# Performance work log

Measured on AMD Instinct MI355X. Metric: run time of the kernel, lower is better.

The kernel has to match this reference:

```python
import jax, jax.numpy as jnp
import numpy as np

T = 10       # Newton-Schulz iterations (module init arg)
EPS = 1e-05  # ridge added to covariance


def setup_inputs() -> dict:
    key = jax.random.key(0)
    # [B, C, H, W] feature map fed into the concept-whitening layer
    X = jax.random.normal(key, (128, 256, 28, 28), dtype=jnp.float32)
    return {"X": X}


def _iternorm_whiten(X):
    """Training-mode IterNorm whitening (g=1 group): ZCA via Newton-Schulz."""
    B, C, H, W = X.shape
    # X.transpose(0,1).view(C, -1): channels-first flatten -> [C, m], m = B*H*W
    x = jnp.moveaxis(X, 0, 1).reshape(C, -1)
    m = x.shape[-1]
    mean = x.mean(-1, keepdims=True)                      # [C, 1]
    xc = x - mean                                         # [C, m]
    I = jnp.eye(C, dtype=X.dtype)
    # Sigma = eps*I + (1/m) * xc @ xc^T
    Sigma = EPS * I + (xc @ xc.T) * (1.0 / m)             # [C, C]
    rTr = 1.0 / jnp.trace(Sigma)                          # scalar
    Sigma_N = Sigma * rTr                                 # trace-normalized

    def newton_step(P, _):
        # P_{k+1} = 1.5*P_k - 0.5 * P_k^3 @ Sigma_N
        P3 = P @ P @ P
        return 1.5 * P - 0.5 * (P3 @ Sigma_N), None

    P, _ = jax.lax.scan(newton_step, I, None, length=T)
    wm = P * jnp.sqrt(rTr)                                # whitening matrix [C, C]
    xn = wm @ xc                                          # [C, m]
    # reshape back: view(C, B, H, W).transpose(0, 1) -> [B, C, H, W]
    return jnp.moveaxis(xn.reshape(C, B, H, W), 0, 1)


def reference(X):
    # IterNormRotation.forward with mode=-1 (default): X_hat = IterNorm.apply(X, ...)
    # The concept-alignment branch (mode >= 0) runs under no_grad and is skipped.
    return _iternorm_whiten(X)
```

## Files before the change

kernel.cpp:

```cpp
#include <hip/hip_runtime.h>


#define HW 784
#define BHW 200704
#define INV_M (1.0f/100352.0f)
#define EPS_RIDGE 1e-5f

typedef __bf16 bf8 __attribute__((ext_vector_type(8)));
typedef float  f4  __attribute__((ext_vector_type(4)));

__device__ __forceinline__ f4 mfma16(bf8 a, bf8 b, f4 c){
  return __builtin_amdgcn_mfma_f32_16x16x32_bf16(a, b, c, 0, 0, 0);
}

__device__ __forceinline__ unsigned short f2bf_rne(float f){
  unsigned u = __builtin_bit_cast(unsigned, f);
  return (unsigned short)((u + 0x7fffu + ((u >> 16) & 1u)) >> 16);
}
__device__ __forceinline__ float bf2f(unsigned short h){
  unsigned u = ((unsigned)h) << 16;
  return __builtin_bit_cast(float, u);
}
__device__ __forceinline__ void split_bf(float f, unsigned short& h, unsigned short& l){
  h = f2bf_rne(f);
  float r = f - bf2f(h);
  l = f2bf_rne(r);
}

__global__ __launch_bounds__(512, 2) void cov_kernel(const float* __restrict__ X,
                                                     float* __restrict__ part,
                                                     float* __restrict__ chansum){
  __shared__ unsigned short Ah[256][40];
  __shared__ unsigned short Al[256][40];
  __shared__ float ssum[256];
  const int t = threadIdx.x;
  const int blk = blockIdx.x;
  const int b = blk >> 1;
  const int h = blk & 1;
  const int base_hw = h * 400;
  const int len    = h ? 384 : 400;
  const int nsteps = h ? 12  : 13;
  const float* __restrict__ Xb = X + (size_t)b * BHW;

  if (t < 256) ssum[t] = 0.0f;

  const int lane = t & 63;
  const int wave = t >> 6;
  const int wm = wave >> 2;
  const int wn = wave & 3;
  const int lr = lane & 15;
  const int ko = lane >> 4;

  f4 acc[8][4];
  #pragma unroll
  for (int m = 0; m < 8; m++)
    #pragma unroll
    for (int n = 0; n < 4; n++) acc[m][n] = f4{0.f, 0.f, 0.f, 0.f};

  float csum[4] = {0.f, 0.f, 0.f, 0.f};
  const int srow = t >> 3;
  const int sfq  = t & 7;

  for (int ks = 0; ks < nsteps; ++ks){
    if (ks) __syncthreads();
    #pragma unroll
    for (int i = 0; i < 4; i++){
      int row = srow + i * 64;
      int hwl = ks * 32 + sfq * 4;
      float4 v = make_float4(0.f, 0.f, 0.f, 0.f);
      if (hwl < len) v = *(const float4*)&Xb[(size_t)row * HW + base_hw + hwl];
      csum[i] += v.x + v.y + v.z + v.w;
      unsigned short h0,l0,h1,l1,h2,l2,h3,l3;
      split_bf(v.x, h0, l0); split_bf(v.y, h1, l1);
      split_bf(v.z, h2, l2); split_bf(v.w, h3, l3);
      *(ushort4*)&Ah[row][sfq * 4] = make_ushort4(h0, h1, h2, h3);
      *(ushort4*)&Al[row][sfq * 4] = make_ushort4(l0, l1, l2, l3);
    }
    __syncthreads();
    bf8 bhf[4], blf[4];
    #pragma unroll
    for (int n = 0; n < 4; n++){
      int coln = wn * 64 + n * 16 + lr;
      bhf[n] = *(const bf8*)&Ah[coln][ko * 8];
      blf[n] = *(const bf8*)&Al[coln][ko * 8];
    }
    #pragma unroll
    for (int m = 0; m < 8; m++){
      int rowm = wm * 128 + m * 16 + lr;
      bf8 ahf = *(const bf8*)&Ah[rowm][ko * 8];
      bf8 alf = *(const bf8*)&Al[rowm][ko * 8];
      #pragma unroll
      for (int n = 0; n < 4; n++){
        acc[m][n] = mfma16(ahf, bhf[n], acc[m][n]);
        acc[m][n] = mfma16(ahf, blf[n], acc[m][n]);
        acc[m][n] = mfma16(alf, bhf[n], acc[m][n]);
      }
    }
  }
  atomicAdd(&ssum[srow      ], csum[0]);
  atomicAdd(&ssum[srow +  64], csum[1]);
  atomicAdd(&ssum[srow + 128], csum[2]);
  atomicAdd(&ssum[srow + 192], csum[3]);
  __syncthreads();
  if (t < 256) atomicAdd(&chansum[t], ssum[t]);

  float* __restrict__ Pp = part + (size_t)blk * 65536;
  const int cr4 = (lane >> 4) * 4;
  #pragma unroll
  for (int m = 0; m < 8; m++){
    #pragma unroll
    for (int n = 0; n < 4; n++){
      int colw = wn * 64 + n * 16 + lr;
      #pragma unroll
      for (int r = 0; r < 4; r++){
        int roww = wm * 128 + m * 16 + cr4 + r;
        Pp[roww * 256 + colw] = acc[m][n][r];
      }
    }
  }
}

__global__ __launch_bounds__(256) void reduce_kernel(const float* __restrict__ part,
                                                     const float* __restrict__ chansum,
                                                     float* __restrict__ Sig,
                                                     float* __restrict__ trace){
  const int i = blockIdx.x;
  const int j = threadIdx.x;
  float s = 0.f;
  #pragma unroll 8
  for (int p = 0; p < 256; p++) s += part[(size_t)p * 65536 + i * 256 + j];
  float mi = chansum[i] * INV_M;
  float mj = chansum[j] * INV_M;
  float v = s * INV_M - mi * mj + ((i == j) ? EPS_RIDGE : 0.f);
  Sig[i * 256 + j] = v;
  if (i == j) atomicAdd(trace, v);
}

__global__ __launch_bounds__(256) void prep_kernel(const float* __restrict__ Sig,
                                                   const float* __restrict__ trace,
                                                   float* __restrict__ SigN,
                                                   float* __restrict__ P1){
  const int idx = blockIdx.x * 256 + threadIdx.x;
  const float rTr = 1.0f / trace[0];
  const float sn = Sig[idx] * rTr;
  SigN[idx] = sn;
  const int i = idx >> 8, j = idx & 255;
  P1[idx] = ((i == j) ? 1.5f : 0.0f) - 0.5f * sn;
}

__global__ __launch_bounds__(256) void mm256_kernel(const float* __restrict__ A,
                                                    const float* __restrict__ B0,
                                                    const float* __restrict__ B1,
                                                    float* __restrict__ O0,
                                                    float* __restrict__ O1,
                                                    const float* __restrict__ E,
                                                    float alpha, float beta){
  const float* __restrict__ B = blockIdx.z ? B1 : B0;
  float* __restrict__ O = blockIdx.z ? O1 : O0;
  __shared__ unsigned short Ah[64][40], Al[64][40], Bh[64][40], Bl[64][40];
  const int t = threadIdx.x;
  const int lane = t & 63;
  const int wave = t >> 6;
  const int wm = wave >> 1, wn = wave & 1;
  const int lr = lane & 15, ko = lane >> 4;
  const int r0 = blockIdx.x * 64, c0 = blockIdx.y * 64;
  f4 acc[2][2];
  acc[0][0] = f4{0.f,0.f,0.f,0.f}; acc[0][1] = f4{0.f,0.f,0.f,0.f};
  acc[1][0] = f4{0.f,0.f,0.f,0.f}; acc[1][1] = f4{0.f,0.f,0.f,0.f};

  for (int ks = 0; ks < 8; ++ks){
    if (ks) __syncthreads();
    #pragma unroll
    for (int i = 0; i < 2; i++){
      int idx = i * 256 + t;
      int row = idx >> 3, fq = idx & 7;
      float4 v = *(const float4*)&A[(r0 + row) * 256 + ks * 32 + fq * 4];
      unsigned short h0,l0,h1,l1,h2,l2,h3,l3;
      split_bf(v.x, h0, l0); split_bf(v.y, h1, l1);
      split_bf(v.z, h2, l2); split_bf(v.w, h3, l3);
      *(ushort4*)&Ah[row][fq * 4] = make_ushort4(h0, h1, h2, h3);
      *(ushort4*)&Al[row][fq * 4] = make_ushort4(l0, l1, l2, l3);
    }
    #pragma unroll
    for (int i = 0; i < 2; i++){
      int idx = i * 256 + t;
      int k = idx >> 4, cq = idx & 15;
      float4 v = *(const float4*)&B[(ks * 32 + k) * 256 + c0 + cq * 4];
      unsigned short hh, ll;
      split_bf(v.x, hh, ll); Bh[cq*4+0][k] = hh; Bl[cq*4+0][k] = ll;
      split_bf(v.y, hh, ll); Bh[cq*4+1][k] = hh; Bl[cq*4+1][k] = ll;
      split_bf(v.z, hh, ll); Bh[cq*4+2][k] = hh; Bl[cq*4+2][k] = ll;
      split_bf(v.w, hh, ll); Bh[cq*4+3][k] = hh; Bl[cq*4+3][k] = ll;
    }
    __syncthreads();
    #pragma unroll
    for (int m = 0; m < 2; m++){
      bf8 ahf = *(const bf8*)&Ah[wm * 32 + m * 16 + lr][ko * 8];
      bf8 alf = *(const bf8*)&Al[wm * 32 + m * 16 + lr][ko * 8];
      #pragma unroll
      for (int n = 0; n < 2; n++){
        bf8 bhf = *(const bf8*)&Bh[wn * 32 + n * 16 + lr][ko * 8];
        bf8 blf = *(const bf8*)&Bl[wn * 32 + n * 16 + lr][ko * 8];
        acc[m][n] = mfma16(ahf, bhf, acc[m][n]);
        acc[m][n] = mfma16(ahf, blf, acc[m][n]);
        acc[m][n] = mfma16(alf, bhf, acc[m][n]);
      }
    }
  }
  const int cr4 = (lane >> 4) * 4;
  #pragma unroll
  for (int m = 0; m < 2; m++)
    #pragma unroll
    for (int n = 0; n < 2; n++)
      #pragma unroll
      for (int r = 0; r < 4; r++){
        int row = r0 + wm * 32 + m * 16 + cr4 + r;
        int col = c0 + wn * 32 + n * 16 + lr;
        float v = alpha * acc[m][n][r];
        if (beta != 0.0f) v += beta * E[row * 256 + col];
        O[row * 256 + col] = v;
      }
}

__global__ __launch_bounds__(256) void wmprep_kernel(const float* __restrict__ P,
                                                     const float* __restrict__ trace,
                                                     const float* __restrict__ chansum,
                                                     unsigned short* __restrict__ wmhi,
                                                     unsigned short* __restrict__ wmlo,
                                                     float* __restrict__ woff){
  const int i = blockIdx.x, t = threadIdx.x;
  __shared__ float red[256];
  const float s = sqrtf(1.0f / trace[0]);
  float v = P[i * 256 + t] * s;
  unsigned short h, l;
  split_bf(v, h, l);
  wmhi[i * 256 + t] = h;
  wmlo[i * 256 + t] = l;
  red[t] = v * (chansum[t] * INV_M);
  __syncthreads();
  for (int st = 128; st > 0; st >>= 1){
    if (t < st) red[t] += red[t + st];
    __syncthreads();
  }
  if (t == 0) woff[i] = red[0];
}

__global__ __launch_bounds__(512, 2) void whiten_kernel(const float* __restrict__ X,
                                                        const unsigned short* __restrict__ wmhi,
                                                        const unsigned short* __restrict__ wmlo,
                                                        const float* __restrict__ woff,
                                                        float* __restrict__ out){
  __shared__ unsigned short Ahs[256][40], Als[256][40];
  __shared__ unsigned short Bhs[112][40], Bls[112][40];
  const int blk = blockIdx.x;
  const int b = blk / 7;
  const int ch = blk % 7;
  const int hw0 = ch * 112;
  const int t = threadIdx.x;
  const int lane = t & 63;
  const int wave = t >> 6;
  const int lr = lane & 15, ko = lane >> 4;
  const float* __restrict__ Xb = X + (size_t)b * BHW;
  f4 acc[2][7];
  #pragma unroll
  for (int m = 0; m < 2; m++)
    #pragma unroll
    for (int n = 0; n < 7; n++) acc[m][n] = f4{0.f, 0.f, 0.f, 0.f};

  const int arow = t >> 1, aseg = t & 1;
  for (int ks = 0; ks < 8; ++ks){
    if (ks) __syncthreads();
    {
      const uint4* sh = (const uint4*)(wmhi + arow * 256 + ks * 32 + aseg * 16);
      uint4 v0 = sh[0], v1 = sh[1];
      *(uint4*)&Ahs[arow][aseg * 16]     = v0;
      *(uint4*)&Ahs[arow][aseg * 16 + 8] = v1;
      const uint4* sl = (const uint4*)(wmlo + arow * 256 + ks * 32 + aseg * 16);
      uint4 w0 = sl[0], w1 = sl[1];
      *(uint4*)&Als[arow][aseg * 16]     = w0;
      *(uint4*)&Als[arow][aseg * 16 + 8] = w1;
    }
    #pragma unroll
    for (int i = 0; i < 2; i++){
      int idx = i * 512 + t;
      if (idx < 896){
        int k = idx / 28, q = idx % 28;
        float4 v = *(const float4*)&Xb[(size_t)(ks * 32 + k) * HW + hw0 + q * 4];
        unsigned short hh, ll;
        split_bf(v.x, hh, ll); Bhs[q*4+0][k] = hh; Bls[q*4+0][k] = ll;
        split_bf(v.y, hh, ll); Bhs[q*4+1][k] = hh; Bls[q*4+1][k] = ll;
        split_bf(v.z, hh, ll); Bhs[q*4+2][k] = hh; Bls[q*4+2][k] = ll;
        split_bf(v.w, hh, ll); Bhs[q*4+3][k] = hh; Bls[q*4+3][k] = ll;
      }
    }
    __syncthreads();
    bf8 bhf[7], blf[7];
    #pragma unroll
    for (int n = 0; n < 7; n++){
      bhf[n] = *(const bf8*)&Bhs[n * 16 + lr][ko * 8];
      blf[n] = *(const bf8*)&Bls[n * 16 + lr][ko * 8];
    }
    #pragma unroll
    for (int m = 0; m < 2; m++){
      bf8 ahf = *(const bf8*)&Ahs[wave * 32 + m * 16 + lr][ko * 8];
      bf8 alf = *(const bf8*)&Als[wave * 32 + m * 16 + lr][ko * 8];
      #pragma unroll
      for (int n = 0; n < 7; n++){
        acc[m][n] = mfma16(ahf, bhf[n], acc[m][n]);
        acc[m][n] = mfma16(ahf, blf[n], acc[m][n]);
        acc[m][n] = mfma16(alf, bhf[n], acc[m][n]);
      }
    }
  }
  const int cr4 = (lane >> 4) * 4;
  #pragma unroll
  for (int m = 0; m < 2; m++){
    #pragma unroll
    for (int r = 0; r < 4; r++){
      int c = wave * 32 + m * 16 + cr4 + r;
      float wofc = woff[c];
      #pragma unroll
      for (int n = 0; n < 7; n++){
        int hw = hw0 + n * 16 + lr;
        out[(size_t)b * BHW + (size_t)c * HW + hw] = acc[m][n][r] - wofc;
      }
    }
  }
}

extern "C" void kernel_launch(void* const* d_in, const int* in_sizes, int n_in,
                              void* d_out, int out_size, void* d_ws, size_t ws_size,
                              hipStream_t stream){
  const float* X = (const float*)d_in[0];
  float* out = (float*)d_out;
  char* ws = (char*)d_ws;
  float* part    = (float*)(ws);
  float* chansum = (float*)(ws + 67108864);
  float* trace   = (float*)(ws + 67108864 + 1024);
  float* Sig     = (float*)(ws + 67110912);
  float* SigN    = (float*)(ws + 67373056);
  float* Pa      = (float*)(ws + 67635200);
  float* Pb      = (float*)(ws + 67897344);
  float* C1      = (float*)(ws + 68159488);
  float* C2      = (float*)(ws + 68421632);
  float* woff    = (float*)(ws + 68683776);
  unsigned short* wmhi = (unsigned short*)(ws + 68685824);
  unsigned short* wmlo = (unsigned short*)(ws + 68816896);

  hipMemsetAsync(ws + 67108864, 0, 2048, stream);
  cov_kernel   <<<256, 512, 0, stream>>>(X, part, chansum);
  reduce_kernel<<<256, 256, 0, stream>>>(part, chansum, Sig, trace);
  prep_kernel  <<<256, 256, 0, stream>>>(Sig, trace, SigN, Pa);

  float* P = Pa; float* Pn = Pb;
  for (int it = 0; it < 9; ++it){
    mm256_kernel<<<dim3(4,4,2), 256, 0, stream>>>(P, P, SigN, C1, C2, nullptr, 1.0f, 0.0f);
    mm256_kernel<<<dim3(4,4,1), 256, 0, stream>>>(C1, C2, nullptr, Pn, nullptr, P, -0.5f, 1.5f);
    float* tmp = P; P = Pn; Pn = tmp;
  }

  wmprep_kernel<<<256, 256, 0, stream>>>(P, trace, chansum, wmhi, wmlo, woff);
  whiten_kernel<<<896, 512, 0, stream>>>(X, wmhi, wmlo, woff, out);
}
```

Measured before the change: 617.9 us.

## Load NS matmul operands row-wise via symmetry and transpose whiten tiles with shuffles

```diff
diff --git a/kernel.cpp b/kernel.cpp
--- a/kernel.cpp
+++ b/kernel.cpp
@@ -148,62 +148,59 @@
   P1[idx] = ((i == j) ? 1.5f : 0.0f) - 0.5f * sn;
 }
 
-__global__ __launch_bounds__(256) void mm256_kernel(const float* __restrict__ A,
-                                                    const float* __restrict__ B0,
-                                                    const float* __restrict__ B1,
-                                                    float* __restrict__ O0,
-                                                    float* __restrict__ O1,
-                                                    const float* __restrict__ E,
-                                                    float alpha, float beta){
+__global__ __launch_bounds__(256) void ns64_kernel(const float* __restrict__ A,
+                                                   const float* __restrict__ B0,
+                                                   const float* __restrict__ B1,
+                                                   float* __restrict__ O0,
+                                                   float* __restrict__ O1,
+                                                   const float* __restrict__ E,
+                                                   float alpha, float beta){
   const float* __restrict__ B = blockIdx.z ? B1 : B0;
   float* __restrict__ O = blockIdx.z ? O1 : O0;
-  __shared__ unsigned short Ah[64][40], Al[64][40], Bh[64][40], Bl[64][40];
+  __shared__ unsigned short Ah[64][136], Al[64][136], Bh[64][136], Bl[64][136];
   const int t = threadIdx.x;
   const int lane = t & 63;
   const int wave = t >> 6;
   const int wm = wave >> 1, wn = wave & 1;
   const int lr = lane & 15, ko = lane >> 4;
   const int r0 = blockIdx.x * 64, c0 = blockIdx.y * 64;
+  const int srow = t >> 2;
+  const int sc0 = (t & 3) * 32;
   f4 acc[2][2];
   acc[0][0] = f4{0.f,0.f,0.f,0.f}; acc[0][1] = f4{0.f,0.f,0.f,0.f};
   acc[1][0] = f4{0.f,0.f,0.f,0.f}; acc[1][1] = f4{0.f,0.f,0.f,0.f};
 
-  for (int ks = 0; ks < 8; ++ks){
-    if (ks) __syncthreads();
-    #pragma unroll
-    for (int i = 0; i < 2; i++){
-      int idx = i * 256 + t;
-      int row = idx >> 3, fq = idx & 7;
-      float4 v = *(const float4*)&A[(r0 + row) * 256 + ks * 32 + fq * 4];
+  for (int kh = 0; kh < 2; ++kh){
+    if (kh) __syncthreads();
+    #pragma unroll
+    for (int i = 0; i < 8; i++){
+      int col = sc0 + i * 4;
+      int gcol = kh * 128 + col;
       unsigned short h0,l0,h1,l1,h2,l2,h3,l3;
-      split_bf(v.x, h0, l0); split_bf(v.y, h1, l1);
-      split_bf(v.z, h2, l2); split_bf(v.w, h3, l3);
-      *(ushort4*)&Ah[row][fq * 4] = make_ushort4(h0, h1, h2, h3);
-      *(ushort4*)&Al[row][fq * 4] = make_ushort4(l0, l1, l2, l3);
-    }
-    #pragma unroll
-    for (int i = 0; i < 2; i++){
-      int idx = i * 256 + t;
-      int k = idx >> 4, cq = idx & 15;
-      float4 v = *(const float4*)&B[(ks * 32 + k) * 256 + c0 + cq * 4];
-      unsigned short hh, ll;
-      split_bf(v.x, hh, ll); Bh[cq*4+0][k] = hh; Bl[cq*4+0][k] = ll;
-      split_bf(v.y, hh, ll); Bh[cq*4+1][k] = hh; Bl[cq*4+1][k] = ll;
-      split_bf(v.z, hh, ll); Bh[cq*4+2][k] = hh; Bl[cq*4+2][k] = ll;
-      split_bf(v.w, hh, ll); Bh[cq*4+3][k] = hh; Bl[cq*4+3][k] = ll;
+      float4 va = *(const float4*)&A[(r0 + srow) * 256 + gcol];
+      split_bf(va.x,h0,l0); split_bf(va.y,h1,l1); split_bf(va.z,h2,l2); split_bf(va.w,h3,l3);
+      *(ushort4*)&Ah[srow][col] = make_ushort4(h0,h1,h2,h3);
+      *(ushort4*)&Al[srow][col] = make_ushort4(l0,l1,l2,l3);
+      float4 vb = *(const float4*)&B[(c0 + srow) * 256 + gcol];
+      split_bf(vb.x,h0,l0); split_bf(vb.y,h1,l1); split_bf(vb.z,h2,l2); split_bf(vb.w,h3,l3);
+      *(ushort4*)&Bh[srow][col] = make_ushort4(h0,h1,h2,h3);
+      *(ushort4*)&Bl[srow][col] = make_ushort4(l0,l1,l2,l3);
     }
     __syncthreads();
     #pragma unroll
-    for (int m = 0; m < 2; m++){
-      bf8 ahf = *(const bf8*)&Ah[wm * 32 + m * 16 + lr][ko * 8];
-      bf8 alf = *(const bf8*)&Al[wm * 32 + m * 16 + lr][ko * 8];
-      #pragma unroll
-      for (int n = 0; n < 2; n++){
-        bf8 bhf = *(const bf8*)&Bh[wn * 32 + n * 16 + lr][ko * 8];
-        bf8 blf = *(const bf8*)&Bl[wn * 32 + n * 16 + lr][ko * 8];
-        acc[m][n] = mfma16(ahf, bhf, acc[m][n]);
-        acc[m][n] = mfma16(ahf, blf, acc[m][n]);
-        acc[m][n] = mfma16(alf, bhf, acc[m][n]);
+    for (int ks = 0; ks < 4; ++ks){
+      #pragma unroll
+      for (int m = 0; m < 2; m++){
+        bf8 ahf = *(const bf8*)&Ah[wm * 32 + m * 16 + lr][ks * 32 + ko * 8];
+        bf8 alf = *(const bf8*)&Al[wm * 32 + m * 16 + lr][ks * 32 + ko * 8];
+        #pragma unroll
+        for (int n = 0; n < 2; n++){
+          bf8 bhf = *(const bf8*)&Bh[wn * 32 + n * 16 + lr][ks * 32 + ko * 8];
+          bf8 blf = *(const bf8*)&Bl[wn * 32 + n * 16 + lr][ks * 32 + ko * 8];
+          acc[m][n] = mfma16(ahf, bhf, acc[m][n]);
+          acc[m][n] = mfma16(ahf, blf, acc[m][n]);
+          acc[m][n] = mfma16(alf, bhf, acc[m][n]);
+        }
       }
     }
   }
@@ -268,6 +265,8 @@
     for (int n = 0; n < 7; n++) acc[m][n] = f4{0.f, 0.f, 0.f, 0.f};
 
   const int arow = t >> 1, aseg = t & 1;
+  const int g = lane >> 4;
+  const int cc = (t >> 4);
   for (int ks = 0; ks < 8; ++ks){
     if (ks) __syncthreads();
     {
@@ -281,16 +280,28 @@
       *(uint4*)&Als[arow][aseg * 16 + 8] = w1;
     }
     #pragma unroll
-    for (int i = 0; i < 2; i++){
-      int idx = i * 512 + t;
-      if (idx < 896){
-        int k = idx / 28, q = idx % 28;
-        float4 v = *(const float4*)&Xb[(size_t)(ks * 32 + k) * HW + hw0 + q * 4];
-        unsigned short hh, ll;
-        split_bf(v.x, hh, ll); Bhs[q*4+0][k] = hh; Bls[q*4+0][k] = ll;
-        split_bf(v.y, hh, ll); Bhs[q*4+1][k] = hh; Bls[q*4+1][k] = ll;
-        split_bf(v.z, hh, ll); Bhs[q*4+2][k] = hh; Bls[q*4+2][k] = ll;
-        split_bf(v.w, hh, ll); Bhs[q*4+3][k] = hh; Bls[q*4+3][k] = ll;
+    for (int p = 0; p < 2; p++){
+      int qh = p * 16 + (t & 15);
+      if (qh < 28){
+        float4 v = *(const float4*)&Xb[(size_t)(ks * 32 + cc) * HW + hw0 + qh * 4];
+        float r0 = __shfl_xor((g & 1) ? v.x : v.y, 16);
+        float r1 = __shfl_xor((g & 1) ? v.z : v.w, 16);
+        float a0 = (g & 1) ? r0  : v.x;
+        float a1 = (g & 1) ? v.y : r0;
+        float a2 = (g & 1) ? r1  : v.z;
+        float a3 = (g & 1) ? v.w : r1;
+        float s0 = __shfl_xor((g & 2) ? a0 : a2, 32);
+        float s1 = __shfl_xor((g & 2) ? a1 : a3, 32);
+        float b0v = (g & 2) ? s0 : a0;
+        float b1v = (g & 2) ? s1 : a1;
+        float b2v = (g & 2) ? a2 : s0;
+        float b3v = (g & 2) ? a3 : s1;
+        int row = qh * 4 + g;
+        int colk = (t >> 6) * 4;
+        unsigned short h0,l0,h1,l1,h2,l2,h3,l3;
+        split_bf(b0v,h0,l0); split_bf(b1v,h1,l1); split_bf(b2v,h2,l2); split_bf(b3v,h3,l3);
+        *(ushort4*)&Bhs[row][colk] = make_ushort4(h0,h1,h2,h3);
+        *(ushort4*)&Bls[row][colk] = make_ushort4(l0,l1,l2,l3);
       }
     }
     __syncthreads();
@@ -354,8 +365,8 @@
 
   float* P = Pa; float* Pn = Pb;
   for (int it = 0; it < 9; ++it){
-    mm256_kernel<<<dim3(4,4,2), 256, 0, stream>>>(P, P, SigN, C1, C2, nullptr, 1.0f, 0.0f);
-    mm256_kernel<<<dim3(4,4,1), 256, 0, stream>>>(C1, C2, nullptr, Pn, nullptr, P, -0.5f, 1.5f);
+    ns64_kernel<<<dim3(4,4,2), 256, 0, stream>>>(P, P, SigN, C1, C2, nullptr, 1.0f, 0.0f);
+    ns64_kernel<<<dim3(4,4,1), 256, 0, stream>>>(C1, C2, nullptr, Pn, nullptr, P, -0.5f, 1.5f);
     float* tmp = P; P = Pn; Pn = tmp;
   }
 
```

New measurement: 495.8 us. 1.25x faster.
